# Kernel tuning notes

Hardware: AMD Instinct MI355X
Metric: run time of the kernel (lower is better)

## Reference

```python
import jax, jax.numpy as jnp
import numpy as np

OUT = 7          # roi_layer out_size
SR = 2           # roi_layer sample_num (sampling ratio)
STRIDES = (4, 8, 16, 32)
FINEST_SCALE = 56.0


def roi_align_level(feat, rois, spatial_scale):
    """RoIAlign (aligned=False, torchvision/mmdet classic) for all rois on one level.
    feat: (B, C, H, W), rois: (K, 5) [batch_idx, x1, y1, x2, y2] in image coords.
    Returns (K, C, OUT, OUT)."""
    B, C, H, W = feat.shape
    b = rois[:, 0].astype(jnp.int32)
    x1 = rois[:, 1] * spatial_scale
    y1 = rois[:, 2] * spatial_scale
    x2 = rois[:, 3] * spatial_scale
    y2 = rois[:, 4] * spatial_scale
    roi_w = jnp.maximum(x2 - x1, 1.0)
    roi_h = jnp.maximum(y2 - y1, 1.0)
    bin_w = roi_w / OUT
    bin_h = roi_h / OUT
    # per-bin sample offsets: (OUT, SR) fractional bin positions
    off = jnp.arange(OUT, dtype=jnp.float32)[:, None] + (jnp.arange(SR, dtype=jnp.float32)[None, :] + 0.5) / SR
    ys = y1[:, None, None] + off[None] * bin_h[:, None, None]   # (K, OUT, SR)
    xs = x1[:, None, None] + off[None] * bin_w[:, None, None]   # (K, OUT, SR)
    y = ys[:, :, :, None, None]                                  # (K, OUT, SR, 1, 1)
    x = xs[:, None, None, :, :]                                  # (K, 1, 1, OUT, SR)
    y, x = jnp.broadcast_arrays(y, x)                            # (K, OUT, SR, OUT, SR)
    valid = (y > -1.0) & (y < H) & (x > -1.0) & (x < W)
    yc = jnp.clip(y, 0.0, H - 1.0)
    xc = jnp.clip(x, 0.0, W - 1.0)
    y0 = jnp.floor(yc)
    x0 = jnp.floor(xc)
    ly = yc - y0
    lx = xc - x0
    hy = 1.0 - ly
    hx = 1.0 - lx
    y0i = y0.astype(jnp.int32)
    x0i = x0.astype(jnp.int32)
    y1i = jnp.minimum(y0i + 1, H - 1)
    x1i = jnp.minimum(x0i + 1, W - 1)
    bb = jnp.broadcast_to(b[:, None, None, None, None], y0i.shape)

    def g(yi, xi):
        # advanced indexing (batched gather) -> (K, OUT, SR, OUT, SR, C)
        return feat[bb, :, yi, xi]

    val = (hy * hx)[..., None] * g(y0i, x0i) \
        + (hy * lx)[..., None] * g(y0i, x1i) \
        + (ly * hx)[..., None] * g(y1i, x0i) \
        + (ly * lx)[..., None] * g(y1i, x1i)
    val = jnp.where(valid[..., None], val, 0.0)
    pooled = val.mean(axis=(2, 4))           # average SRxSR samples -> (K, OUT, OUT, C)
    return jnp.transpose(pooled, (0, 3, 1, 2))  # (K, C, OUT, OUT)


def map_roi_levels(rois, num_levels):
    scale = jnp.sqrt((rois[:, 3] - rois[:, 1] + 1.0) * (rois[:, 4] - rois[:, 2] + 1.0))
    lvl = jnp.floor(jnp.log2(scale / FINEST_SCALE + 1e-6))
    return jnp.clip(lvl, 0, num_levels - 1).astype(jnp.int32)


def setup_inputs() -> dict:
    key = jax.random.key(0)
    ks = jax.random.split(key, 10)
    B, C = 2, 256
    IMG_H, IMG_W = 800.0, 1344.0
    feats = {}
    shapes = [(B, C, 200, 336), (B, C, 100, 168), (B, C, 50, 84), (B, C, 25, 42)]
    for i, s in enumerate(shapes):
        feats[f"feat{i}"] = jax.random.normal(ks[i], s, dtype=jnp.float32)
    K = 1024
    bidx = jax.random.randint(ks[4], (K,), 0, B).astype(jnp.float32)
    # log-uniform box sizes in [16, ~724] px so all 4 FPN levels get rois
    w = 2.0 ** jax.random.uniform(ks[5], (K,), minval=4.0, maxval=9.5)
    h = 2.0 ** jax.random.uniform(ks[6], (K,), minval=4.0, maxval=9.5)
    cx = jax.random.uniform(ks[7], (K,), minval=0.0, maxval=IMG_W)
    cy = jax.random.uniform(ks[8], (K,), minval=0.0, maxval=IMG_H)
    x1 = jnp.clip(cx - w * 0.5, 0.0, IMG_W - 2.0)
    y1 = jnp.clip(cy - h * 0.5, 0.0, IMG_H - 2.0)
    x2 = jnp.clip(x1 + w, x1 + 1.0, IMG_W - 1.0)
    y2 = jnp.clip(y1 + h, y1 + 1.0, IMG_H - 1.0)
    rois = jnp.stack([bidx, x1, y1, x2, y2], axis=-1).astype(jnp.float32)
    feats["rois"] = rois
    return feats


def reference(feat0, feat1, feat2, feat3, rois):
    feats = [feat0, feat1, feat2, feat3]
    num_levels = len(feats)
    target_lvls = map_roi_levels(rois, num_levels)
    K = rois.shape[0]
    C = feats[0].shape[1]
    roi_feats = jnp.zeros((K, C, OUT, OUT), dtype=feats[0].dtype)
    for i in range(num_levels):
        ri = roi_align_level(feats[i], rois, 1.0 / STRIDES[i])
        mask = (target_lvls == i)[:, None, None, None]
        roi_feats = roi_feats + jnp.where(mask, ri, 0.0)
    return roi_feats
```

## Files before the change

kernel.cpp:

```cpp
#include <hip/hip_runtime.h>
#include <stdint.h>
#include <stddef.h>

#define C_TOTAL     256
#define CPG         4
#define NGROUPS     (C_TOTAL / CPG)
#define NBINS       49
#define NSAMP       196
#define MAX_CELLS   1664
#define TILE_STRIDE (MAX_CELLS + 64)

__global__ __launch_bounds__(256, 4)
void roi_align_fused(const float* __restrict__ f0,
                     const float* __restrict__ f1,
                     const float* __restrict__ f2,
                     const float* __restrict__ f3,
                     const float* __restrict__ rois,
                     float* __restrict__ out)
{
    __shared__ float  s_tile[CPG * TILE_STRIDE];
    __shared__ float4 s_w4[NSAMP];
    __shared__ int4   s_c4[NSAMP];

    const int k    = blockIdx.y;
    const int g    = blockIdx.x;
    const int tid  = threadIdx.x;
    const int wv   = tid >> 6;
    const int lane = tid & 63;

    const float bf  = rois[k * 5 + 0];
    const float rx1 = rois[k * 5 + 1];
    const float ry1 = rois[k * 5 + 2];
    const float rx2 = rois[k * 5 + 3];
    const float ry2 = rois[k * 5 + 4];
    const int   b   = (int)bf;

    const float scale = sqrtf((rx2 - rx1 + 1.0f) * (ry2 - ry1 + 1.0f));
    int lvl = (int)floorf(log2f(scale / 56.0f + 1e-6f));
    lvl = lvl < 0 ? 0 : (lvl > 3 ? 3 : lvl);

    const float* feat; int H, W;
    if      (lvl == 0) { feat = f0; H = 200; W = 336; }
    else if (lvl == 1) { feat = f1; H = 100; W = 168; }
    else if (lvl == 2) { feat = f2; H =  50; W =  84; }
    else               { feat = f3; H =  25; W =  42; }

    const float ss  = 1.0f / (float)(4 << lvl);
    const float x1s = rx1 * ss, y1s = ry1 * ss;
    const float x2s = rx2 * ss, y2s = ry2 * ss;
    const float roi_w = fmaxf(x2s - x1s, 1.0f);
    const float roi_h = fmaxf(y2s - y1s, 1.0f);
    const float bw = roi_w * (1.0f / 7.0f);
    const float bh = roi_h * (1.0f / 7.0f);

    const float Hm1 = (float)(H - 1), Wm1 = (float)(W - 1);
    const int ty0 = (int)floorf(fminf(fmaxf(y1s + 0.25f * bh, 0.0f), Hm1));
    const int tx0 = (int)floorf(fminf(fmaxf(x1s + 0.25f * bw, 0.0f), Wm1));
    const int ty1 = min((int)floorf(fminf(fmaxf(y1s + 6.75f * bh, 0.0f), Hm1)) + 1, H - 1);
    const int tx1 = min((int)floorf(fminf(fmaxf(x1s + 6.75f * bw, 0.0f), Wm1)) + 1, W - 1);
    const int fh = ty1 - ty0 + 1;
    const int fw = tx1 - tx0 + 1;
    int cells = fh * fw;
    cells = cells > MAX_CELLS ? MAX_CELLS : cells;

    {
        const int c = g * CPG + wv;
        const float* src = feat + ((size_t)(b * C_TOTAL + c) * (size_t)H + (size_t)ty0) * (size_t)W + tx0;
        float* dst = s_tile + wv * TILE_STRIDE;
        for (int base = 0; base < cells; base += 64) {
            int cell = base + lane;
            cell = cell < cells ? cell : (cells - 1);
            const int fy = (int)((unsigned)cell / (unsigned)fw);
            const int fx = cell - fy * fw;
            __builtin_amdgcn_global_load_lds(
                (const __attribute__((address_space(1))) uint32_t*)(src + (size_t)fy * W + fx),
                (__attribute__((address_space(3))) uint32_t*)(dst + base),
                4, 0, 0);
        }
    }

    if (tid < NSAMP) {
        const int iy = tid / 14;
        const int ix = tid - iy * 14;
        const float yy = y1s + ((float)iy * 0.5f + 0.25f) * bh;
        const float xx = x1s + ((float)ix * 0.5f + 0.25f) * bw;
        const bool valid = (yy > -1.0f) && (yy < (float)H) && (xx > -1.0f) && (xx < (float)W);
        const float yc  = fminf(fmaxf(yy, 0.0f), Hm1);
        const float xc  = fminf(fmaxf(xx, 0.0f), Wm1);
        const float y0f = floorf(yc);
        const float x0f = floorf(xc);
        const float ly = yc - y0f, lx = xc - x0f;
        const float hy = 1.0f - ly, hx = 1.0f - lx;
        const int y0  = (int)y0f, x0 = (int)x0f;
        const int y1i = min(y0 + 1, H - 1);
        const int x1i = min(x0 + 1, W - 1);
        const int ry0 = y0  - ty0, ry1b = y1i - ty0;
        const int rx0 = x0  - tx0, rx1b = x1i - tx0;
        const float v = valid ? 0.25f : 0.0f;
        s_w4[tid] = make_float4(hy * hx * v, hy * lx * v, ly * hx * v, ly * lx * v);
        s_c4[tid] = make_int4(ry0 * fw + rx0, ry0 * fw + rx1b,
                              ry1b * fw + rx0, ry1b * fw + rx1b);
    }

    asm volatile("s_waitcnt vmcnt(0)" ::: "memory");
    __syncthreads();

    if (lane < NBINS) {
        const float* t = s_tile + wv * TILE_STRIDE;
        const int oy = lane / 7;
        const int ox = lane - oy * 7;
        const int sbase = oy * 28 + ox * 2;
        float acc = 0.0f;
#pragma unroll
        for (int sy = 0; sy < 2; ++sy) {
#pragma unroll
            for (int sx = 0; sx < 2; ++sx) {
                const int s = sbase + sy * 14 + sx;
                const float4 w = s_w4[s];
                const int4   cc = s_c4[s];
                acc += w.x * t[cc.x] + w.y * t[cc.y]
                     + w.z * t[cc.z] + w.w * t[cc.w];
            }
        }
        const int c = g * CPG + wv;
        out[((size_t)k * C_TOTAL + c) * NBINS + lane] = acc;
    }
}

extern "C" void kernel_launch(void* const* d_in, const int* in_sizes, int n_in,
                              void* d_out, int out_size, void* d_ws, size_t ws_size,
                              hipStream_t stream) {
    const float* f0   = (const float*)d_in[0];
    const float* f1   = (const float*)d_in[1];
    const float* f2   = (const float*)d_in[2];
    const float* f3   = (const float*)d_in[3];
    const float* rois = (const float*)d_in[4];
    float* out = (float*)d_out;

    const int K = in_sizes[4] / 5;
    dim3 grid(NGROUPS, K, 1);
    roi_align_fused<<<grid, 256, 0, stream>>>(f0, f1, f2, f3, rois, out);
}
```

Baseline: 162.7 us.

## Use 16-byte LDS-direct tile loads and compute bilinear weights per lane

Feature tile staging now uses 16-byte global_load_lds chunks aligned to 4-float boundaries, falling back to 4-byte loads for level 3 or for tiles that exceed the buffer. It also replaces the per-element integer division with a multiply-shift reciprocal and overlaps the last partial chunk instead of clamping lanes. The shared sample weight and offset tables are removed: each lane recomputes its own bilinear weights and indices, which shrinks LDS use and allows occupancy to rise from 4 to 5 blocks. The cost is extra per-lane arithmetic, plus wider fetches that load some redundant columns.

```diff
diff --git a/kernel.cpp b/kernel.cpp
--- a/kernel.cpp
+++ b/kernel.cpp
@@ -6,11 +6,10 @@
 #define CPG         4
 #define NGROUPS     (C_TOTAL / CPG)
 #define NBINS       49
-#define NSAMP       196
-#define MAX_CELLS   1664
-#define TILE_STRIDE (MAX_CELLS + 64)
+#define TILE_D      1920
+#define CHUNK16_MAX (TILE_D / 4)
 
-__global__ __launch_bounds__(256, 4)
+__global__ __launch_bounds__(256, 5)
 void roi_align_fused(const float* __restrict__ f0,
                      const float* __restrict__ f1,
                      const float* __restrict__ f2,
@@ -18,9 +17,7 @@
                      const float* __restrict__ rois,
                      float* __restrict__ out)
 {
-    __shared__ float  s_tile[CPG * TILE_STRIDE];
-    __shared__ float4 s_w4[NSAMP];
-    __shared__ int4   s_c4[NSAMP];
+    __shared__ __align__(16) float s_tile[CPG * TILE_D];
 
     const int k    = blockIdx.y;
     const int g    = blockIdx.x;
@@ -60,66 +57,90 @@
     const int tx1 = min((int)floorf(fminf(fmaxf(x1s + 6.75f * bw, 0.0f), Wm1)) + 1, W - 1);
     const int fh = ty1 - ty0 + 1;
     const int fw = tx1 - tx0 + 1;
-    int cells = fh * fw;
-    cells = cells > MAX_CELLS ? MAX_CELLS : cells;
+
+    int cpr = (fw + (tx0 & 3) + 3) >> 2;
+    if (cpr > (W >> 2)) cpr = W >> 2;
+    const bool use16 = (lvl < 3) && (fh * cpr <= CHUNK16_MAX);
+
+    int rb, rowStride, chunks;
+    if (use16) {
+        rb = tx0 & ~3;
+        if (rb + 4 * cpr > W) rb = W - 4 * cpr;
+        rowStride = 4 * cpr;
+        chunks = fh * cpr;
+    } else {
+        rb = tx0;
+        rowStride = fw;
+        chunks = fh * fw;
+        if (chunks > TILE_D) chunks = TILE_D;
+    }
+    const uint32_t d = use16 ? (uint32_t)cpr : (uint32_t)fw;
+    const uint32_t M = (1u << 22) / d + 1u;
+    const int dW = W - rowStride;
 
     {
         const int c = g * CPG + wv;
-        const float* src = feat + ((size_t)(b * C_TOTAL + c) * (size_t)H + (size_t)ty0) * (size_t)W + tx0;
-        float* dst = s_tile + wv * TILE_STRIDE;
-        for (int base = 0; base < cells; base += 64) {
-            int cell = base + lane;
-            cell = cell < cells ? cell : (cells - 1);
-            const int fy = (int)((unsigned)cell / (unsigned)fw);
-            const int fx = cell - fy * fw;
-            __builtin_amdgcn_global_load_lds(
-                (const __attribute__((address_space(1))) uint32_t*)(src + (size_t)fy * W + fx),
-                (__attribute__((address_space(3))) uint32_t*)(dst + base),
-                4, 0, 0);
+        const float* src = feat + ((size_t)(b * C_TOTAL + c) * (size_t)H + (size_t)ty0) * (size_t)W + rb;
+        float* dst = s_tile + wv * TILE_D;
+        if (use16) {
+            for (int start = 0; start < chunks; start += 64) {
+                int s = (start + 64 > chunks) ? max(chunks - 64, 0) : start;
+                int idx = s + lane;
+                if (idx >= chunks) idx = chunks - 1;
+                const int fy = (int)(((uint32_t)idx * M) >> 22);
+                const int off = (idx << 2) + fy * dW;
+                __builtin_amdgcn_global_load_lds(
+                    (const __attribute__((address_space(1))) uint32_t*)(src + off),
+                    (__attribute__((address_space(3))) uint32_t*)(dst + (s << 2)),
+                    16, 0, 0);
+            }
+        } else {
+            for (int start = 0; start < chunks; start += 64) {
+                int s = (start + 64 > chunks) ? max(chunks - 64, 0) : start;
+                int idx = s + lane;
+                if (idx >= chunks) idx = chunks - 1;
+                const int fy = (int)(((uint32_t)idx * M) >> 22);
+                const int off = idx + fy * dW;
+                __builtin_amdgcn_global_load_lds(
+                    (const __attribute__((address_space(1))) uint32_t*)(src + off),
+                    (__attribute__((address_space(3))) uint32_t*)(dst + s),
+                    4, 0, 0);
+            }
         }
-    }
-
-    if (tid < NSAMP) {
-        const int iy = tid / 14;
-        const int ix = tid - iy * 14;
-        const float yy = y1s + ((float)iy * 0.5f + 0.25f) * bh;
-        const float xx = x1s + ((float)ix * 0.5f + 0.25f) * bw;
-        const bool valid = (yy > -1.0f) && (yy < (float)H) && (xx > -1.0f) && (xx < (float)W);
-        const float yc  = fminf(fmaxf(yy, 0.0f), Hm1);
-        const float xc  = fminf(fmaxf(xx, 0.0f), Wm1);
-        const float y0f = floorf(yc);
-        const float x0f = floorf(xc);
-        const float ly = yc - y0f, lx = xc - x0f;
-        const float hy = 1.0f - ly, hx = 1.0f - lx;
-        const int y0  = (int)y0f, x0 = (int)x0f;
-        const int y1i = min(y0 + 1, H - 1);
-        const int x1i = min(x0 + 1, W - 1);
-        const int ry0 = y0  - ty0, ry1b = y1i - ty0;
-        const int rx0 = x0  - tx0, rx1b = x1i - tx0;
-        const float v = valid ? 0.25f : 0.0f;
-        s_w4[tid] = make_float4(hy * hx * v, hy * lx * v, ly * hx * v, ly * lx * v);
-        s_c4[tid] = make_int4(ry0 * fw + rx0, ry0 * fw + rx1b,
-                              ry1b * fw + rx0, ry1b * fw + rx1b);
     }
 
     asm volatile("s_waitcnt vmcnt(0)" ::: "memory");
     __syncthreads();
 
     if (lane < NBINS) {
-        const float* t = s_tile + wv * TILE_STRIDE;
+        const float* t = s_tile + wv * TILE_D;
         const int oy = lane / 7;
         const int ox = lane - oy * 7;
-        const int sbase = oy * 28 + ox * 2;
+        const float Hf = (float)H, Wf = (float)W;
         float acc = 0.0f;
 #pragma unroll
         for (int sy = 0; sy < 2; ++sy) {
 #pragma unroll
             for (int sx = 0; sx < 2; ++sx) {
-                const int s = sbase + sy * 14 + sx;
-                const float4 w = s_w4[s];
-                const int4   cc = s_c4[s];
-                acc += w.x * t[cc.x] + w.y * t[cc.y]
-                     + w.z * t[cc.z] + w.w * t[cc.w];
+                const float yy = y1s + ((float)oy + 0.25f + 0.5f * (float)sy) * bh;
+                const float xx = x1s + ((float)ox + 0.25f + 0.5f * (float)sx) * bw;
+                const bool valid = (yy > -1.0f) && (yy < Hf) && (xx > -1.0f) && (xx < Wf);
+                const float yc  = fminf(fmaxf(yy, 0.0f), Hm1);
+                const float xc  = fminf(fmaxf(xx, 0.0f), Wm1);
+                const float y0f = floorf(yc);
+                const float x0f = floorf(xc);
+                const float ly = yc - y0f, lx = xc - x0f;
+                const float hy = 1.0f - ly, hx = 1.0f - lx;
+                const int y0  = (int)y0f, x0 = (int)x0f;
+                const int y1i = min(y0 + 1, H - 1);
+                const int x1i = min(x0 + 1, W - 1);
+                const int r0 = (y0  - ty0) * rowStride - rb;
+                const int r1 = (y1i - ty0) * rowStride - rb;
+                const float v = valid ? 0.25f : 0.0f;
+                acc += (hy * hx * v) * t[r0 + x0]
+                     + (hy * lx * v) * t[r0 + x1i]
+                     + (ly * hx * v) * t[r1 + x0]
+                     + (ly * lx * v) * t[r1 + x1i];
             }
         }
         const int c = g * CPG + wv;
```

Measured after the change: 147.1 us. -9.6%, faster.
